# Kernel tuning notes

Hardware: AMD Instinct MI355X
Metric: run time of the kernel (lower is better)

Reference implementation:

```python
import jax, jax.numpy as jnp
import numpy as np

B, N, C, H = 2, 2048, 128, 4
C4 = C // 4


def setup_inputs() -> dict:
    key = jax.random.key(0)
    ks = jax.random.split(key, 20)
    s = 0.02
    f = lambda k, sh: (jax.random.normal(k, sh, jnp.float32) * s)
    return {
        'x': jax.random.normal(ks[0], (B, N, C), jnp.float32),
        'A': jax.random.randint(ks[1], (N, N), 0, 2).astype(jnp.int32),
        'q_w1': f(ks[2], (C, C)), 'kv_w1': f(ks[3], (2 * C, C)),
        'proj_w1': f(ks[4], (C, C)), 'proj_b1': jnp.zeros((C,), jnp.float32),
        'q_w2': f(ks[5], (C, C)), 'kv_w2': f(ks[6], (2 * C, C)),
        'proj_w2': f(ks[7], (C, C)), 'proj_b2': jnp.zeros((C,), jnp.float32),
        'cq_w': f(ks[8], (C4, C)), 'cq_b': jnp.zeros((C4,), jnp.float32),
        'ck_w': f(ks[9], (C4, C)), 'ck_b': jnp.zeros((C4,), jnp.float32),
        'cv_w': f(ks[10], (C, C)), 'cv_b': jnp.zeros((C,), jnp.float32),
        'gc_w': f(ks[11], (C, C)), 'gc_b': jnp.zeros((C,), jnp.float32),
    }


def _attn_block(x, A, qw, kvw, pw, pb):
    # Attention._inner_attention + residual; qkv_bias=False, scale=head_dim**-0.5
    b, n, c = x.shape
    hd = c // H
    q = (x @ qw.T).reshape(b, n, H, hd).transpose(0, 2, 1, 3)          # [B,H,N,hd]
    kv = (x @ kvw.T).reshape(b, n, 2, H, hd).transpose(2, 0, 3, 1, 4)  # [2,B,H,N,hd]
    k, v = kv[0], kv[1]
    attn = jnp.einsum('bhnd,bhmd->bhnm', q, k) * (hd ** -0.5)
    attn = jnp.where(A[None, None] > 0, attn, jnp.float32(-9e15))
    attn = jax.nn.softmax(attn, axis=-1)
    out = jnp.einsum('bhnm,bhmd->bhnd', attn, v).transpose(0, 2, 1, 3).reshape(b, n, c)
    return out @ pw.T + pb + x


def _graph_conv(x, cq_w, cq_b, ck_w, ck_b, cv_w, cv_b, gc_w, gc_b):
    # GraphConvolution.forward: conv1d(k=1) QKV, softmax, topk scatter mask, masked softmax, bmm
    b, s, c = x.shape
    xp = x.transpose(0, 2, 1)                                          # [B,C,N]
    query = jnp.einsum('oi,bin->bon', cq_w, xp) + cq_b[:, None]        # [B,C/4,N]
    keyt = (jnp.einsum('oi,bin->bon', ck_w, xp) + ck_b[:, None]).transpose(0, 2, 1)  # [B,N,C/4]
    adj = jax.nn.softmax(jnp.einsum('bnc,bcm->bnm', keyt, query), axis=-1)           # [B,N,N]
    kk = int(s / 3 * 2)                                                # top-2/3 per row
    _, idx = jax.lax.top_k(adj, kk)                                    # [B,N,kk]
    mask = jnp.zeros(adj.shape, bool).at[
        jnp.arange(b)[:, None, None], jnp.arange(s)[None, :, None], idx].set(True)
    adj = jax.nn.softmax(jnp.where(mask, adj, -jnp.inf), axis=-1)
    value = (jnp.einsum('oi,bin->bon', cv_w, xp) + cv_b[:, None]).transpose(0, 2, 1)  # [B,N,C]
    support = value @ gc_w
    return jnp.einsum('bnm,bmc->bnc', adj, support) + gc_b


def reference(x, A, q_w1, kv_w1, proj_w1, proj_b1, q_w2, kv_w2, proj_w2, proj_b2,
              cq_w, cq_b, ck_w, ck_b, cv_w, cv_b, gc_w, gc_b):
    x = _attn_block(x, A, q_w1, kv_w1, proj_w1, proj_b1)
    x = _attn_block(x, A, q_w2, kv_w2, proj_w2, proj_b2)
    return _graph_conv(x, cq_w, cq_b, ck_w, ck_b, cv_w, cv_b, gc_w, gc_b)
```

## Files before the change

kernel.cpp:

```cpp
#include <hip/hip_runtime.h>
#include <hip/hip_bf16.h>
#include <math.h>

#define BB 2
#define NN 2048
#define CC 128
#define HH 4
#define HD 32
#define KK_TOP 1365

typedef __attribute__((ext_vector_type(8))) short v8s;
typedef __attribute__((ext_vector_type(4))) float f32x4;

#define MFMA16(a, b, c) __builtin_amdgcn_mfma_f32_16x16x32_bf16(a, b, c, 0, 0, 0)

__device__ inline float wave_max_f(float v) {
    #pragma unroll
    for (int m = 1; m < 64; m <<= 1) v = fmaxf(v, __shfl_xor(v, m));
    return v;
}
__device__ inline float wave_min_f(float v) {
    #pragma unroll
    for (int m = 1; m < 64; m <<= 1) v = fminf(v, __shfl_xor(v, m));
    return v;
}
__device__ inline float wave_sum_f(float v) {
    #pragma unroll
    for (int m = 1; m < 64; m <<= 1) v += __shfl_xor(v, m);
    return v;
}
__device__ inline unsigned short bf16bits(float x) {
    __hip_bfloat16 h = __float2bfloat16(x);
    return *reinterpret_cast<unsigned short*>(&h);
}

__global__ __launch_bounds__(256) void prep_k(
    const int* __restrict__ A, unsigned* __restrict__ Ab2,
    const float* __restrict__ cv_w, const float* __restrict__ cv_b,
    const float* __restrict__ gc_w, float* __restrict__ MT, float* __restrict__ B2)
{
    const int bx = blockIdx.x;
    if (bx < 512) {
        const int lane = threadIdx.x & 63;
        const int w = threadIdx.x >> 6;
        const int row = bx * 4 + w;
        const int* rp = A + (size_t)row * 2048;
        for (int i = 0; i < 32; ++i) {
            unsigned long long bal = __ballot(rp[i * 64 + lane] > 0);
            if (lane == 0)  Ab2[(size_t)row * 64 + 2 * i]     = (unsigned)bal;
            if (lane == 32) Ab2[(size_t)row * 64 + 2 * i + 1] = (unsigned)(bal >> 32);
        }
    } else {
        const int b2 = bx - 512;
        const int c = b2 * 2 + (threadIdx.x >> 7);
        const int k = threadIdx.x & 127;
        float a = 0.f;
        #pragma unroll 4
        for (int i = 0; i < 128; ++i)
            a += cv_w[(size_t)i * 128 + k] * gc_w[(size_t)i * 128 + c];
        MT[(size_t)c * 128 + k] = a;
        if (b2 == 0 && threadIdx.x < 128) {
            float s = 0.f;
            #pragma unroll 4
            for (int i = 0; i < 128; ++i)
                s += cv_b[i] * gc_w[(size_t)i * 128 + threadIdx.x];
            B2[threadIdx.x] = s;
        }
    }
}

enum { MODE_QKV = 0, MODE_PROJ = 1 };

template <int MODE>
__global__ __launch_bounds__(256) void gemm128_k(
    const float* __restrict__ X, const float* __restrict__ W0,
    const float* __restrict__ W1, const float* __restrict__ bias,
    const float* __restrict__ resid, void* __restrict__ out0v,
    void* __restrict__ out1v, void* __restrict__ out2v)
{
    __shared__ __align__(16) float Xs[64][132];
    __shared__ __align__(16) float Ws[32][132];
    const int tid = threadIdx.x;
    const int m0 = blockIdx.x * 64;
    const int n0 = blockIdx.y * 32;

    #pragma unroll
    for (int i = 0; i < 32; ++i) {
        int idx = tid + i * 256;
        int row = idx >> 7, col = idx & 127;
        Xs[row][col] = X[(size_t)(m0 + row) * 128 + col];
    }
    #pragma unroll
    for (int i = 0; i < 16; ++i) {
        int idx = tid + i * 256;
        int r = idx >> 7, col = idx & 127;
        int gr = n0 + r;
        const float* wp;
        if (MODE == MODE_QKV)
            wp = (gr < 128) ? (W0 + (size_t)gr * 128) : (W1 + (size_t)(gr - 128) * 128);
        else
            wp = W0 + (size_t)gr * 128;
        Ws[r][col] = wp[col];
    }
    __syncthreads();

    const int r = tid >> 4;
    const int c = tid & 15;
    float acc[4][2] = {{0.f, 0.f}, {0.f, 0.f}, {0.f, 0.f}, {0.f, 0.f}};

    #pragma unroll
    for (int k = 0; k < 128; k += 4) {
        float4 w0 = *(const float4*)&Ws[c][k];
        float4 w1 = *(const float4*)&Ws[c + 16][k];
        #pragma unroll
        for (int i = 0; i < 4; ++i) {
            float4 xv = *(const float4*)&Xs[r + 16 * i][k];
            acc[i][0] += xv.x * w0.x + xv.y * w0.y + xv.z * w0.z + xv.w * w0.w;
            acc[i][1] += xv.x * w1.x + xv.y * w1.y + xv.z * w1.z + xv.w * w1.w;
        }
    }

    #pragma unroll
    for (int i = 0; i < 4; ++i) {
        int m = m0 + r + 16 * i;
        int b = m >> 11, n = m & 2047;
        #pragma unroll
        for (int jj = 0; jj < 2; ++jj) {
            int ccol = n0 + c + 16 * jj;
            float v = acc[i][jj];
            if (MODE == MODE_QKV) {
                __hip_bfloat16 hv = __float2bfloat16(v);
                if (ccol < 128) {
                    int hh = ccol >> 5, d = ccol & 31;
                    ((__hip_bfloat16*)out0v)[((size_t)(b * 4 + hh) * 2048 + n) * 32 + d] = hv;
                } else if (ccol < 256) {
                    int c2 = ccol - 128; int hh = c2 >> 5, d = c2 & 31;
                    ((__hip_bfloat16*)out1v)[((size_t)(b * 4 + hh) * 2048 + n) * 32 + d] = hv;
                } else {
                    int c2 = ccol - 256; int hh = c2 >> 5, d = c2 & 31;
                    ((__hip_bfloat16*)out2v)[((size_t)(b * 4 + hh) * 32 + d) * 2048 + n] = hv;
                }
            } else {
                ((float*)out0v)[(size_t)m * 128 + ccol] = v + bias[ccol] + resid[(size_t)m * 128 + ccol];
            }
        }
    }
}

__global__ __launch_bounds__(256) void graphmm_k(
    const float* __restrict__ X, const float* __restrict__ cq_w,
    const float* __restrict__ cq_b, const float* __restrict__ ck_w,
    const float* __restrict__ ck_b, const float* __restrict__ MT,
    const float* __restrict__ B2, float* __restrict__ QgT,
    float* __restrict__ Kg, __hip_bfloat16* __restrict__ SUPt)
{
    __shared__ __align__(16) float Xs[64][132];
    __shared__ __align__(16) float Ws[32][132];
    const int tid = threadIdx.x;
    const int m0 = blockIdx.x * 64;
    const int y = blockIdx.y;
    const float* W0   = (y == 0) ? cq_w : (y == 1) ? ck_w : MT;
    const float* bias = (y == 0) ? cq_b : (y == 1) ? ck_b : B2;
    const int n0 = (y < 2) ? 0 : (y - 2) * 32;

    #pragma unroll
    for (int i = 0; i < 32; ++i) {
        int idx = tid + i * 256;
        int row = idx >> 7, col = idx & 127;
        Xs[row][col] = X[(size_t)(m0 + row) * 128 + col];
    }
    #pragma unroll
    for (int i = 0; i < 16; ++i) {
        int idx = tid + i * 256;
        int r = idx >> 7, col = idx & 127;
        Ws[r][col] = W0[(size_t)(n0 + r) * 128 + col];
    }
    __syncthreads();

    const int r = tid >> 4;
    const int c = tid & 15;
    float acc[4][2] = {{0.f, 0.f}, {0.f, 0.f}, {0.f, 0.f}, {0.f, 0.f}};

    #pragma unroll
    for (int k = 0; k < 128; k += 4) {
        float4 w0 = *(const float4*)&Ws[c][k];
        float4 w1 = *(const float4*)&Ws[c + 16][k];
        #pragma unroll
        for (int i = 0; i < 4; ++i) {
            float4 xv = *(const float4*)&Xs[r + 16 * i][k];
            acc[i][0] += xv.x * w0.x + xv.y * w0.y + xv.z * w0.z + xv.w * w0.w;
            acc[i][1] += xv.x * w1.x + xv.y * w1.y + xv.z * w1.z + xv.w * w1.w;
        }
    }

    #pragma unroll
    for (int i = 0; i < 4; ++i) {
        int m = m0 + r + 16 * i;
        int b = m >> 11, n = m & 2047;
        #pragma unroll
        for (int jj = 0; jj < 2; ++jj) {
            int ccol = n0 + c + 16 * jj;
            float v = acc[i][jj];
            if (y == 0) {
                QgT[((size_t)b * 32 + ccol) * 2048 + n] = v + bias[ccol];
            } else if (y == 1) {
                Kg[(size_t)m * 32 + ccol] = v + bias[ccol];
            } else {
                SUPt[((size_t)b * 128 + ccol) * 2048 + n] = __float2bfloat16(v + bias[ccol]);
            }
        }
    }
}

__global__ __launch_bounds__(512, 8) void attn_mfma_k(
    const short* __restrict__ Qb, const short* __restrict__ Kb,
    const short* __restrict__ Vt, const unsigned* __restrict__ Ab2,
    float* __restrict__ O)
{
    __shared__ __align__(16) float OLDS[8][64][8];
    __shared__ float lred[8][16];

    const int tid = threadIdx.x;
    const int w = tid >> 6, lane = tid & 63;
    const int g = lane >> 4, c = lane & 15;
    const int bb = 4 * g;
    const int wg = blockIdx.x;
    const int b = wg >> 9, h = (wg >> 7) & 3, r0w = (wg & 127) << 4;
    const int bh = b * 4 + h;

    const v8s qf = *(const v8s*)(Qb + ((size_t)bh * 2048 + r0w + c) * 32 + g * 8);
    const short* Kp = Kb + (size_t)bh * 2048 * 32;
    const short* Vp = Vt + (size_t)bh * 32 * 2048;
    const unsigned* Mrow = Ab2 + (size_t)(r0w + c) * 64;

    f32x4 o0 = {0.f, 0.f, 0.f, 0.f}, o1 = {0.f, 0.f, 0.f, 0.f};
    float lsum = 0.f;
    const float SC2 = 0.25503487f;
    const bool lo = (g < 2);
    const int aA = (32 * (g & 1) + c) * 4;
    const int aB = aA + 64;

    #pragma unroll 2
    for (int t = 0; t < 8; ++t) {
        const int kt = t * 8 + w;
        const int key0 = kt * 32;
        v8s kf0 = *(const v8s*)(Kp + (size_t)(key0 + c) * 32 + g * 8);
        v8s kf1 = *(const v8s*)(Kp + (size_t)(key0 + 16 + c) * 32 + g * 8);
        unsigned mw = Mrow[kt];
        const f32x4 z = {0.f, 0.f, 0.f, 0.f};
        f32x4 s0 = MFMA16(kf0, qf, z);
        f32x4 s1 = MFMA16(kf1, qf, z);

        float p0[4], p1[4];
        #pragma unroll
        for (int r = 0; r < 4; ++r) {
            p0[r] = ((mw >> (bb + r)) & 1u)      ? exp2f(s0[r] * SC2) : 0.f;
            p1[r] = ((mw >> (16 + bb + r)) & 1u) ? exp2f(s1[r] * SC2) : 0.f;
        }
        lsum += p0[0] + p0[1] + p0[2] + p0[3] + p1[0] + p1[1] + p1[2] + p1[3];

        int w00 = (int)bf16bits(p0[0]) | ((int)bf16bits(p0[1]) << 16);
        int w01 = (int)bf16bits(p0[2]) | ((int)bf16bits(p0[3]) << 16);
        int w10 = (int)bf16bits(p1[0]) | ((int)bf16bits(p1[1]) << 16);
        int w11 = (int)bf16bits(p1[2]) | ((int)bf16bits(p1[3]) << 16);

        int e0, e1;
        union { int wv[4]; v8s v; } pf;
        e0 = __builtin_amdgcn_ds_bpermute(aA, w00);
        e1 = __builtin_amdgcn_ds_bpermute(aA, w10);
        pf.wv[0] = lo ? e0 : e1;
        e0 = __builtin_amdgcn_ds_bpermute(aA, w01);
        e1 = __builtin_amdgcn_ds_bpermute(aA, w11);
        pf.wv[1] = lo ? e0 : e1;
        e0 = __builtin_amdgcn_ds_bpermute(aB, w00);
        e1 = __builtin_amdgcn_ds_bpermute(aB, w10);
        pf.wv[2] = lo ? e0 : e1;
        e0 = __builtin_amdgcn_ds_bpermute(aB, w01);
        e1 = __builtin_amdgcn_ds_bpermute(aB, w11);
        pf.wv[3] = lo ? e0 : e1;

        v8s vf0 = *(const v8s*)(Vp + (size_t)c * 2048 + key0 + g * 8);
        v8s vf1 = *(const v8s*)(Vp + (size_t)(16 + c) * 2048 + key0 + g * 8);
        o0 = MFMA16(pf.v, vf0, o0);
        o1 = MFMA16(pf.v, vf1, o1);
    }

    lsum += __shfl_xor(lsum, 16);
    lsum += __shfl_xor(lsum, 32);

    *(f32x4*)&OLDS[w][lane][0] = o0;
    *(f32x4*)&OLDS[w][lane][4] = o1;
    if (lane < 16) lred[w][lane] = lsum;
    __syncthreads();

    if (tid < 64) {
        float iv[4];
        #pragma unroll
        for (int r = 0; r < 4; ++r) {
            float s = lred[0][bb + r];
            #pragma unroll
            for (int ww = 1; ww < 8; ++ww) s += lred[ww][bb + r];
            iv[r] = 1.f / s;
        }
        f32x4 a0 = *(f32x4*)&OLDS[0][lane][0];
        f32x4 a1 = *(f32x4*)&OLDS[0][lane][4];
        #pragma unroll
        for (int ww = 1; ww < 8; ++ww) {
            a0 += *(f32x4*)&OLDS[ww][lane][0];
            a1 += *(f32x4*)&OLDS[ww][lane][4];
        }
        #pragma unroll
        for (int r = 0; r < 4; ++r) {
            size_t base = ((size_t)b * 2048 + r0w + bb + r) * 128 + h * 32;
            O[base + c]      = a0[r] * iv[r];
            O[base + 16 + c] = a1[r] * iv[r];
        }
    }
}

__global__ __launch_bounds__(512, 8) void gadjtopk_k(
    const float* __restrict__ Kg, const float* __restrict__ QgT,
    __hip_bfloat16* __restrict__ ADJb)
{
    __shared__ float kg_s[4][32];
    __shared__ float scores[4][2048];
    __shared__ float redm[4][4], reds[4][4];

    const int tid = threadIdx.x;
    const int wg = blockIdx.x;
    const int b = wg >> 9;
    const int r0 = (wg & 511) << 2;

    if (tid < 128) {
        int rr = tid >> 5, d = tid & 31;
        kg_s[rr][d] = Kg[((size_t)b * 2048 + r0 + rr) * 32 + d];
    }
    __syncthreads();

    const float* Qp = QgT + (size_t)b * 32 * 2048;
    float acc[4][4];
    #pragma unroll
    for (int rr = 0; rr < 4; ++rr)
        #pragma unroll
        for (int s = 0; s < 4; ++s) acc[rr][s] = 0.f;

    #pragma unroll 4
    for (int dd = 0; dd < 32; ++dd) {
        float q0 = kg_s[0][dd], q1 = kg_s[1][dd], q2 = kg_s[2][dd], q3 = kg_s[3][dd];
        const float* kp = Qp + (size_t)dd * 2048 + tid;
        #pragma unroll
        for (int s = 0; s < 4; ++s) {
            float kv = kp[s * 512];
            acc[0][s] = fmaf(q0, kv, acc[0][s]);
            acc[1][s] = fmaf(q1, kv, acc[1][s]);
            acc[2][s] = fmaf(q2, kv, acc[2][s]);
            acc[3][s] = fmaf(q3, kv, acc[3][s]);
        }
    }
    #pragma unroll
    for (int s = 0; s < 4; ++s) {
        int jj = tid + 512 * s;
        #pragma unroll
        for (int rr = 0; rr < 4; ++rr) scores[rr][jj] = acc[rr][s];
    }
    __syncthreads();

    const int lane = tid & 63, wid = tid >> 6;

    if (tid < 256) {
        #pragma unroll
        for (int rr = 0; rr < 4; ++rr) {
            float m = -3.0e38f;
            #pragma unroll
            for (int s = 0; s < 8; ++s) m = fmaxf(m, scores[rr][tid + 256 * s]);
            m = wave_max_f(m);
            if (lane == 0) redm[rr][wid] = m;
        }
    }
    __syncthreads();

    if (tid < 256) {
        float mx[4];
        #pragma unroll
        for (int rr = 0; rr < 4; ++rr)
            mx[rr] = fmaxf(fmaxf(redm[rr][0], redm[rr][1]), fmaxf(redm[rr][2], redm[rr][3]));
        #pragma unroll
        for (int rr = 0; rr < 4; ++rr) {
            float sm = 0.f;
            #pragma unroll
            for (int s = 0; s < 8; ++s) {
                int jj = tid + 256 * s;
                float p = expf(scores[rr][jj] - mx[rr]);
                scores[rr][jj] = p;
                sm += p;
            }
            sm = wave_sum_f(sm);
            if (lane == 0) reds[rr][wid] = sm;
        }
    }
    __syncthreads();

    if (tid < 256) {
        const float ivw = 1.f / (reds[wid][0] + reds[wid][1] + reds[wid][2] + reds[wid][3]);
        unsigned k_[32];
        float mxp = 0.f, mnp = 3.0e38f;
        #pragma unroll
        for (int i = 0; i < 32; ++i) {
            float p = scores[wid][lane + i * 64] * ivw;
            k_[i] = __float_as_uint(p);
            mxp = fmaxf(mxp, p);
            mnp = fminf(mnp, p);
        }
        mxp = wave_max_f(mxp);
        mnp = wave_min_f(mnp);

        unsigned thr = __float_as_uint(mnp);
        const unsigned umax = __float_as_uint(mxp);
        const unsigned diff = thr ^ umax;
        if (diff != 0u) {
            const int hb = 31 - __builtin_clz(diff);
            thr = (umax >> (hb + 1)) << (hb + 1);
            for (int bit = hb; bit >= 0; --bit) {
                unsigned cand = thr | (1u << bit);
                int cnt = 0;
                #pragma unroll
                for (int i = 0; i < 32; ++i)
                    cnt += (int)__popcll(__ballot(k_[i] >= cand));
                if (cnt >= KK_TOP) thr = cand;
            }
        }

        int gt_c = 0;
        #pragma unroll
        for (int i = 0; i < 32; ++i)
            gt_c += (int)__popcll(__ballot(k_[i] > thr));
        const int need = KK_TOP - gt_c;

        unsigned keepmask = 0u;
        int running = 0;
        const unsigned long long ltmask = (lane == 0) ? 0ull : (~0ull >> (64 - lane));
        #pragma unroll
        for (int i = 0; i < 32; ++i) {
            bool tie = (k_[i] == thr);
            unsigned long long bal = __ballot(tie);
            int before = running + (int)__popcll(bal & ltmask);
            bool keep = (k_[i] > thr) || (tie && before < need);
            running += (int)__popcll(bal);
            if (keep) keepmask |= (1u << i);
        }

        const float LOG2E = 1.4426950408889634f;
        float sm = 0.f;
        #pragma unroll
        for (int i = 0; i < 32; ++i)
            if ((keepmask >> i) & 1u)
                sm += exp2f((__uint_as_float(k_[i]) - mxp) * LOG2E);
        sm = wave_sum_f(sm);
        const float ivs = 1.f / sm;

        __hip_bfloat16* rp = ADJb + (size_t)(b * 2048 + r0 + wid) * 2048;
        #pragma unroll
        for (int i = 0; i < 32; ++i) {
            float o = ((keepmask >> i) & 1u)
                        ? exp2f((__uint_as_float(k_[i]) - mxp) * LOG2E) * ivs : 0.f;
            rp[lane + i * 64] = __float2bfloat16(o);
        }
    }
}

__global__ __launch_bounds__(256) void outgemm_mfma_k(
    const short* __restrict__ ADJb, const short* __restrict__ SUPt,
    const float* __restrict__ gcb, float* __restrict__ OUT)
{
    __shared__ __align__(16) float OL[4][64][16];
    const int tid = threadIdx.x;
    const int w = tid >> 6, lane = tid & 63;
    const int g = lane >> 4, c = lane & 15;
    const int r0w = blockIdx.x * 16;
    const int n0 = blockIdx.y * 64;
    const int b = r0w >> 11;
    const short* Bp = SUPt + (size_t)b * 128 * 2048;

    f32x4 acc[4];
    #pragma unroll
    for (int f = 0; f < 4; ++f) acc[f] = (f32x4){0.f, 0.f, 0.f, 0.f};

    #pragma unroll 2
    for (int i = 0; i < 16; ++i) {
        const int k0 = w * 512 + i * 32;
        v8s af = *(const v8s*)(ADJb + (size_t)(r0w + c) * 2048 + k0 + g * 8);
        #pragma unroll
        for (int f = 0; f < 4; ++f) {
            v8s bf_ = *(const v8s*)(Bp + (size_t)(n0 + f * 16 + c) * 2048 + k0 + g * 8);
            acc[f] = MFMA16(af, bf_, acc[f]);
        }
    }

    #pragma unroll
    for (int f = 0; f < 4; ++f) *(f32x4*)&OL[w][lane][f * 4] = acc[f];
    __syncthreads();

    #pragma unroll
    for (int u = 0; u < 4; ++u) {
        int idx = tid + u * 256;
        int ls = idx >> 4, s = idx & 15;
        float v = OL[0][ls][s] + OL[1][ls][s] + OL[2][ls][s] + OL[3][ls][s];
        int f = s >> 2, r = s & 3;
        int row = r0w + 4 * (ls >> 4) + r;
        int col = n0 + f * 16 + (ls & 15);
        OUT[(size_t)row * 128 + col] = v + gcb[col];
    }
}

extern "C" void kernel_launch(void* const* d_in, const int* in_sizes, int n_in,
                              void* d_out, int out_size, void* d_ws, size_t ws_size,
                              hipStream_t stream)
{
    const float* x       = (const float*)d_in[0];
    const int*   A       = (const int*)d_in[1];
    const float* q_w1    = (const float*)d_in[2];
    const float* kv_w1   = (const float*)d_in[3];
    const float* proj_w1 = (const float*)d_in[4];
    const float* proj_b1 = (const float*)d_in[5];
    const float* q_w2    = (const float*)d_in[6];
    const float* kv_w2   = (const float*)d_in[7];
    const float* proj_w2 = (const float*)d_in[8];
    const float* proj_b2 = (const float*)d_in[9];
    const float* cq_w    = (const float*)d_in[10];
    const float* cq_b    = (const float*)d_in[11];
    const float* ck_w    = (const float*)d_in[12];
    const float* ck_b    = (const float*)d_in[13];
    const float* cv_w    = (const float*)d_in[14];
    const float* cv_b    = (const float*)d_in[15];
    const float* gc_w    = (const float*)d_in[16];
    const float* gc_b    = (const float*)d_in[17];
    float* out = (float*)d_out;

    char* ws = (char*)d_ws;
    __hip_bfloat16* Qb   = (__hip_bfloat16*)(ws + 0);
    __hip_bfloat16* Kb   = (__hip_bfloat16*)(ws + 1048576);
    __hip_bfloat16* Vt   = (__hip_bfloat16*)(ws + 2097152);
    __hip_bfloat16* ADJb = (__hip_bfloat16*)(ws + 3145728);
    unsigned*       Ab2  = (unsigned*)      (ws + 19922944);
    float*          O    = (float*)         (ws + 20447232);
    float*          X1   = (float*)         (ws + 22544384);
    float*          X2   = (float*)         (ws + 24641536);
    float*          QgT  = (float*)         (ws + 26738688);
    float*          Kg   = (float*)         (ws + 27262976);
    __hip_bfloat16* SUPt = (__hip_bfloat16*)(ws + 27787264);
    float*          MT   = (float*)         (ws + 28835840);
    float*          B2   = (float*)         (ws + 28901376);

    dim3 blk(256);
    dim3 blk512(512);

    hipLaunchKernelGGL(prep_k, dim3(576), blk, 0, stream, A, Ab2, cv_w, cv_b, gc_w, MT, B2);

    hipLaunchKernelGGL((gemm128_k<MODE_QKV>), dim3(64, 12), blk, 0, stream,
                       x, q_w1, kv_w1, nullptr, nullptr, Qb, Kb, Vt);
    hipLaunchKernelGGL(attn_mfma_k, dim3(1024), blk512, 0, stream,
                       (const short*)Qb, (const short*)Kb, (const short*)Vt, Ab2, O);
    hipLaunchKernelGGL((gemm128_k<MODE_PROJ>), dim3(64, 4), blk, 0, stream,
                       O, proj_w1, nullptr, proj_b1, x, X1, nullptr, nullptr);

    hipLaunchKernelGGL((gemm128_k<MODE_QKV>), dim3(64, 12), blk, 0, stream,
                       X1, q_w2, kv_w2, nullptr, nullptr, Qb, Kb, Vt);
    hipLaunchKernelGGL(attn_mfma_k, dim3(1024), blk512, 0, stream,
                       (const short*)Qb, (const short*)Kb, (const short*)Vt, Ab2, O);
    hipLaunchKernelGGL((gemm128_k<MODE_PROJ>), dim3(64, 4), blk, 0, stream,
                       O, proj_w2, nullptr, proj_b2, X1, X2, nullptr, nullptr);

    hipLaunchKernelGGL(graphmm_k, dim3(64, 6), blk, 0, stream,
                       X2, cq_w, cq_b, ck_w, ck_b, MT, B2, QgT, Kg, SUPt);
    hipLaunchKernelGGL(gadjtopk_k, dim3(1024), blk512, 0, stream, Kg, QgT, ADJb);
    hipLaunchKernelGGL(outgemm_mfma_k, dim3(256, 2), blk, 0, stream,
                       (const short*)ADJb, (const short*)SUPt, gc_b, out);
}
```

Before: 296.9 us.

## Process eight rows per block in top-k kernel and widen output GEMM split-K

The graph adjacency top-k kernel now handles 8 rows per 512-thread block, one row per wave. This removes the idle half of the threads and the cross-wave reductions and barriers for softmax max and sum. The radix threshold search exits early once the count exactly equals k. The output GEMM now uses 8 waves with split-K over 256 columns each, at the cost of a larger LDS reduction buffer. Both kernels use more registers and shared memory per block, which may lower occupancy.

```diff
diff --git a/kernel.cpp b/kernel.cpp
--- a/kernel.cpp
+++ b/kernel.cpp
@@ -318,161 +318,140 @@
     }
 }
 
-__global__ __launch_bounds__(512, 8) void gadjtopk_k(
+__global__ __launch_bounds__(512, 4) void gadjtopk_k(
     const float* __restrict__ Kg, const float* __restrict__ QgT,
     __hip_bfloat16* __restrict__ ADJb)
 {
-    __shared__ float kg_s[4][32];
-    __shared__ float scores[4][2048];
-    __shared__ float redm[4][4], reds[4][4];
+    __shared__ float kg_s[8][32];
+    __shared__ float scores[8][2048];
 
     const int tid = threadIdx.x;
     const int wg = blockIdx.x;
-    const int b = wg >> 9;
-    const int r0 = (wg & 511) << 2;
-
-    if (tid < 128) {
+    const int b = wg >> 8;
+    const int r0 = (wg & 255) << 3;
+
+    if (tid < 256) {
         int rr = tid >> 5, d = tid & 31;
         kg_s[rr][d] = Kg[((size_t)b * 2048 + r0 + rr) * 32 + d];
     }
     __syncthreads();
 
     const float* Qp = QgT + (size_t)b * 32 * 2048;
-    float acc[4][4];
-    #pragma unroll
-    for (int rr = 0; rr < 4; ++rr)
+    float acc[8][4];
+    #pragma unroll
+    for (int rr = 0; rr < 8; ++rr)
         #pragma unroll
         for (int s = 0; s < 4; ++s) acc[rr][s] = 0.f;
 
-    #pragma unroll 4
     for (int dd = 0; dd < 32; ++dd) {
-        float q0 = kg_s[0][dd], q1 = kg_s[1][dd], q2 = kg_s[2][dd], q3 = kg_s[3][dd];
+        float qv[8];
+        #pragma unroll
+        for (int rr = 0; rr < 8; ++rr) qv[rr] = kg_s[rr][dd];
         const float* kp = Qp + (size_t)dd * 2048 + tid;
         #pragma unroll
         for (int s = 0; s < 4; ++s) {
             float kv = kp[s * 512];
-            acc[0][s] = fmaf(q0, kv, acc[0][s]);
-            acc[1][s] = fmaf(q1, kv, acc[1][s]);
-            acc[2][s] = fmaf(q2, kv, acc[2][s]);
-            acc[3][s] = fmaf(q3, kv, acc[3][s]);
+            #pragma unroll
+            for (int rr = 0; rr < 8; ++rr)
+                acc[rr][s] = fmaf(qv[rr], kv, acc[rr][s]);
         }
     }
     #pragma unroll
     for (int s = 0; s < 4; ++s) {
         int jj = tid + 512 * s;
         #pragma unroll
-        for (int rr = 0; rr < 4; ++rr) scores[rr][jj] = acc[rr][s];
+        for (int rr = 0; rr < 8; ++rr) scores[rr][jj] = acc[rr][s];
     }
     __syncthreads();
 
-    const int lane = tid & 63, wid = tid >> 6;
-
-    if (tid < 256) {
-        #pragma unroll
-        for (int rr = 0; rr < 4; ++rr) {
-            float m = -3.0e38f;
+    const int lane = tid & 63, w = tid >> 6;
+
+    float mx = -3.0e38f;
+    #pragma unroll
+    for (int i = 0; i < 32; ++i) mx = fmaxf(mx, scores[w][lane + i * 64]);
+    mx = wave_max_f(mx);
+
+    float sm0 = 0.f;
+    #pragma unroll
+    for (int i = 0; i < 32; ++i) {
+        float p = expf(scores[w][lane + i * 64] - mx);
+        scores[w][lane + i * 64] = p;
+        sm0 += p;
+    }
+    sm0 = wave_sum_f(sm0);
+    const float ivw = 1.f / sm0;
+
+    unsigned k_[32];
+    float mxp = 0.f, mnp = 3.0e38f;
+    #pragma unroll
+    for (int i = 0; i < 32; ++i) {
+        float p = scores[w][lane + i * 64] * ivw;
+        k_[i] = __float_as_uint(p);
+        mxp = fmaxf(mxp, p);
+        mnp = fminf(mnp, p);
+    }
+    mxp = wave_max_f(mxp);
+    mnp = wave_min_f(mnp);
+
+    unsigned thr = __float_as_uint(mnp);
+    const unsigned umax = __float_as_uint(mxp);
+    const unsigned diff = thr ^ umax;
+    if (diff != 0u) {
+        const int hb = 31 - __builtin_clz(diff);
+        thr = (umax >> (hb + 1)) << (hb + 1);
+        for (int bit = hb; bit >= 0; --bit) {
+            unsigned cand = thr | (1u << bit);
+            int cnt = 0;
             #pragma unroll
-            for (int s = 0; s < 8; ++s) m = fmaxf(m, scores[rr][tid + 256 * s]);
-            m = wave_max_f(m);
-            if (lane == 0) redm[rr][wid] = m;
-        }
-    }
-    __syncthreads();
-
-    if (tid < 256) {
-        float mx[4];
-        #pragma unroll
-        for (int rr = 0; rr < 4; ++rr)
-            mx[rr] = fmaxf(fmaxf(redm[rr][0], redm[rr][1]), fmaxf(redm[rr][2], redm[rr][3]));
-        #pragma unroll
-        for (int rr = 0; rr < 4; ++rr) {
-            float sm = 0.f;
-            #pragma unroll
-            for (int s = 0; s < 8; ++s) {
-                int jj = tid + 256 * s;
-                float p = expf(scores[rr][jj] - mx[rr]);
-                scores[rr][jj] = p;
-                sm += p;
-            }
-            sm = wave_sum_f(sm);
-            if (lane == 0) reds[rr][wid] = sm;
-        }
-    }
-    __syncthreads();
-
-    if (tid < 256) {
-        const float ivw = 1.f / (reds[wid][0] + reds[wid][1] + reds[wid][2] + reds[wid][3]);
-        unsigned k_[32];
-        float mxp = 0.f, mnp = 3.0e38f;
-        #pragma unroll
-        for (int i = 0; i < 32; ++i) {
-            float p = scores[wid][lane + i * 64] * ivw;
-            k_[i] = __float_as_uint(p);
-            mxp = fmaxf(mxp, p);
-            mnp = fminf(mnp, p);
-        }
-        mxp = wave_max_f(mxp);
-        mnp = wave_min_f(mnp);
-
-        unsigned thr = __float_as_uint(mnp);
-        const unsigned umax = __float_as_uint(mxp);
-        const unsigned diff = thr ^ umax;
-        if (diff != 0u) {
-            const int hb = 31 - __builtin_clz(diff);
-            thr = (umax >> (hb + 1)) << (hb + 1);
-            for (int bit = hb; bit >= 0; --bit) {
-                unsigned cand = thr | (1u << bit);
-                int cnt = 0;
-                #pragma unroll
-                for (int i = 0; i < 32; ++i)
-                    cnt += (int)__popcll(__ballot(k_[i] >= cand));
-                if (cnt >= KK_TOP) thr = cand;
-            }
-        }
-
-        int gt_c = 0;
-        #pragma unroll
-        for (int i = 0; i < 32; ++i)
-            gt_c += (int)__popcll(__ballot(k_[i] > thr));
-        const int need = KK_TOP - gt_c;
-
-        unsigned keepmask = 0u;
-        int running = 0;
-        const unsigned long long ltmask = (lane == 0) ? 0ull : (~0ull >> (64 - lane));
-        #pragma unroll
-        for (int i = 0; i < 32; ++i) {
-            bool tie = (k_[i] == thr);
-            unsigned long long bal = __ballot(tie);
-            int before = running + (int)__popcll(bal & ltmask);
-            bool keep = (k_[i] > thr) || (tie && before < need);
-            running += (int)__popcll(bal);
-            if (keep) keepmask |= (1u << i);
-        }
-
-        const float LOG2E = 1.4426950408889634f;
-        float sm = 0.f;
-        #pragma unroll
-        for (int i = 0; i < 32; ++i)
-            if ((keepmask >> i) & 1u)
-                sm += exp2f((__uint_as_float(k_[i]) - mxp) * LOG2E);
-        sm = wave_sum_f(sm);
-        const float ivs = 1.f / sm;
-
-        __hip_bfloat16* rp = ADJb + (size_t)(b * 2048 + r0 + wid) * 2048;
-        #pragma unroll
-        for (int i = 0; i < 32; ++i) {
-            float o = ((keepmask >> i) & 1u)
-                        ? exp2f((__uint_as_float(k_[i]) - mxp) * LOG2E) * ivs : 0.f;
-            rp[lane + i * 64] = __float2bfloat16(o);
-        }
-    }
-}
-
-__global__ __launch_bounds__(256) void outgemm_mfma_k(
+            for (int i = 0; i < 32; ++i)
+                cnt += (int)__popcll(__ballot(k_[i] >= cand));
+            if (cnt == KK_TOP) { thr = cand; break; }
+            if (cnt > KK_TOP) thr = cand;
+        }
+    }
+
+    int gt_c = 0;
+    #pragma unroll
+    for (int i = 0; i < 32; ++i)
+        gt_c += (int)__popcll(__ballot(k_[i] > thr));
+    const int need = KK_TOP - gt_c;
+
+    unsigned keepmask = 0u;
+    int running = 0;
+    const unsigned long long ltmask = (lane == 0) ? 0ull : (~0ull >> (64 - lane));
+    #pragma unroll
+    for (int i = 0; i < 32; ++i) {
+        bool tie = (k_[i] == thr);
+        unsigned long long bal = __ballot(tie);
+        int before = running + (int)__popcll(bal & ltmask);
+        bool keep = (k_[i] > thr) || (tie && before < need);
+        running += (int)__popcll(bal);
+        if (keep) keepmask |= (1u << i);
+    }
+
+    const float LOG2E = 1.4426950408889634f;
+    float sm = 0.f;
+    #pragma unroll
+    for (int i = 0; i < 32; ++i)
+        if ((keepmask >> i) & 1u)
+            sm += exp2f((__uint_as_float(k_[i]) - mxp) * LOG2E);
+    sm = wave_sum_f(sm);
+    const float ivs = 1.f / sm;
+
+    __hip_bfloat16* rp = ADJb + (size_t)(b * 2048 + r0 + w) * 2048;
+    #pragma unroll
+    for (int i = 0; i < 32; ++i) {
+        float o = ((keepmask >> i) & 1u)
+                    ? exp2f((__uint_as_float(k_[i]) - mxp) * LOG2E) * ivs : 0.f;
+        rp[lane + i * 64] = __float2bfloat16(o);
+    }
+}
+
+__global__ __launch_bounds__(512, 8) void outgemm_mfma_k(
     const short* __restrict__ ADJb, const short* __restrict__ SUPt,
     const float* __restrict__ gcb, float* __restrict__ OUT)
 {
-    __shared__ __align__(16) float OL[4][64][16];
+    __shared__ __align__(16) float OL[8][64][16];
     const int tid = threadIdx.x;
     const int w = tid >> 6, lane = tid & 63;
     const int g = lane >> 4, c = lane & 15;
@@ -486,8 +465,8 @@
     for (int f = 0; f < 4; ++f) acc[f] = (f32x4){0.f, 0.f, 0.f, 0.f};
 
     #pragma unroll 2
-    for (int i = 0; i < 16; ++i) {
-        const int k0 = w * 512 + i * 32;
+    for (int i = 0; i < 8; ++i) {
+        const int k0 = w * 256 + i * 32;
         v8s af = *(const v8s*)(ADJb + (size_t)(r0w + c) * 2048 + k0 + g * 8);
         #pragma unroll
         for (int f = 0; f < 4; ++f) {
@@ -501,10 +480,12 @@
     __syncthreads();
 
     #pragma unroll
-    for (int u = 0; u < 4; ++u) {
-        int idx = tid + u * 256;
+    for (int u = 0; u < 2; ++u) {
+        int idx = tid + u * 512;
         int ls = idx >> 4, s = idx & 15;
-        float v = OL[0][ls][s] + OL[1][ls][s] + OL[2][ls][s] + OL[3][ls][s];
+        float v = OL[0][ls][s];
+        #pragma unroll
+        for (int ww = 1; ww < 8; ++ww) v += OL[ww][ls][s];
         int f = s >> 2, r = s & 3;
         int row = r0w + 4 * (ls >> 4) + r;
         int col = n0 + f * 16 + (ls & 15);
@@ -572,7 +553,7 @@
 
     hipLaunchKernelGGL(graphmm_k, dim3(64, 6), blk, 0, stream,
                        X2, cq_w, cq_b, ck_w, ck_b, MT, B2, QgT, Kg, SUPt);
-    hipLaunchKernelGGL(gadjtopk_k, dim3(1024), blk512, 0, stream, Kg, QgT, ADJb);
-    hipLaunchKernelGGL(outgemm_mfma_k, dim3(256, 2), blk, 0, stream,
+    hipLaunchKernelGGL(gadjtopk_k, dim3(512), blk512, 0, stream, Kg, QgT, ADJb);
+    hipLaunchKernelGGL(outgemm_mfma_k, dim3(256, 2), blk512, 0, stream,
                        (const short*)ADJb, (const short*)SUPt, gc_b, out);
 }
```

Result: faster. 286.6 us (-3.5%).
